# Performance work log

Measured on AMD Instinct MI355X. Metric: run time of the kernel, lower is better.

## Reference

```python
import jax, jax.numpy as jnp
import numpy as np

V, G, F, T = 500000, 25000, 256, 2


def setup_inputs() -> dict:
    key = jax.random.key(0)
    ks = jax.random.split(key, 10)
    s = 1.0 / np.sqrt(F)
    node_feats = jax.random.normal(ks[0], (V, F), jnp.float32)
    seg_ids = jnp.sort(jax.random.randint(ks[1], (V,), 0, G, dtype=jnp.int32))
    Wl = jax.random.uniform(ks[2], (T, 1, 2 * F), jnp.float32, -s, s)
    bl = jax.random.uniform(ks[3], (T, 1), jnp.float32, -s, s)
    Wp = jax.random.uniform(ks[4], (T, F, F), jnp.float32, -s, s)
    bp = jax.random.uniform(ks[5], (T, F), jnp.float32, -s, s)
    Wih = jax.random.uniform(ks[6], (T, 3 * F, F), jnp.float32, -s, s)
    Whh = jax.random.uniform(ks[7], (T, 3 * F, F), jnp.float32, -s, s)
    bih = jax.random.uniform(ks[8], (T, 3 * F), jnp.float32, -s, s)
    bhh = jax.random.uniform(ks[9], (T, 3 * F), jnp.float32, -s, s)
    return dict(node_feats=node_feats, seg_ids=seg_ids, Wl=Wl, bl=bl,
                Wp=Wp, bp=bp, Wih=Wih, Whh=Whh, bih=bih, bhh=bhh)


def _segment_softmax(z, seg):
    # z: (V,) per-node logits; softmax within each graph segment
    m = jax.ops.segment_max(z, seg, num_segments=G)
    m = jnp.where(jnp.isfinite(m), m, 0.0)  # guard empty segments
    e = jnp.exp(z - m[seg])
    d = jax.ops.segment_sum(e, seg, num_segments=G)
    return e / d[seg]


def _gru_cell(x, h, Wih, Whh, bih, bhh):
    # torch.nn.GRUCell semantics
    gi = x @ Wih.T + bih  # (G, 3F)
    gh = h @ Whh.T + bhh
    ir, iz, inn = jnp.split(gi, 3, axis=1)
    hr, hz, hn = jnp.split(gh, 3, axis=1)
    r = jax.nn.sigmoid(ir + hr)
    zg = jax.nn.sigmoid(iz + hz)
    n = jnp.tanh(inn + r * hn)
    return (1.0 - zg) * n + zg * h


def reference(node_feats, seg_ids, Wl, bl, Wp, bp, Wih, Whh, bih, bhh):
    # initial graph feats = sum of node feats per graph
    g_feats = jax.ops.segment_sum(node_feats, seg_ids, num_segments=G)  # (G, F)
    for t in range(T):
        ctx_in = jnp.concatenate([jax.nn.relu(g_feats)[seg_ids], node_feats], axis=1)  # (V, 2F)
        z = jax.nn.leaky_relu(ctx_in @ Wl[t].T + bl[t], 0.01)[:, 0]  # (V,)
        a = _segment_softmax(z, seg_ids)[:, None]  # (V, 1)
        hv = node_feats @ Wp[t].T + bp[t]  # dropout=0 -> identity
        g_repr = jax.ops.segment_sum(a * hv, seg_ids, num_segments=G)  # (G, F)
        context = jax.nn.elu(g_repr)
        g_feats = _gru_cell(context, g_feats, Wih[t], Whh[t], bih[t], bhh[t])
    return g_feats
```

## Files before the change

kernel.cpp:

```cpp
#include <hip/hip_runtime.h>
#include <cstdint>

typedef unsigned short u16;
typedef unsigned int u32;

#define V_N 500000
#define G_N 25000
#define F_N 256
#define GP_N 25088

typedef __attribute__((ext_vector_type(8))) __bf16 bf16x8;
typedef __attribute__((ext_vector_type(4))) float f32x4;

__device__ __forceinline__ u16 f2bf(float f) {
  u32 u = __builtin_bit_cast(u32, f);
  u += 0x7fffu + ((u >> 16) & 1u);
  return (u16)(u >> 16);
}
__device__ __forceinline__ float bf2f(u16 s) {
  u32 u = ((u32)s) << 16;
  return __builtin_bit_cast(float, u);
}
__device__ __forceinline__ float sigm(float x) { return 1.f / (1.f + __expf(-x)); }
__device__ __forceinline__ float tanh_fast(float x) {
  return 1.f - 2.f / (__expf(2.f * x) + 1.f);
}
__device__ __forceinline__ float lrelu(float z) { return z >= 0.f ? z : 0.01f * z; }

__device__ __forceinline__ void load_lds16(const void* g, void* l) {
  __builtin_amdgcn_global_load_lds(
      (const __attribute__((address_space(1))) void*)g,
      (__attribute__((address_space(3))) void*)l, 16, 0, 0);
}

__global__ __launch_bounds__(256) void k_convw(const float* __restrict__ Wp,
                                               const float* __restrict__ Wih,
                                               const float* __restrict__ Whh,
                                               u16* __restrict__ Wpb, u16* __restrict__ W3) {
  int i = blockIdx.x * 256 + threadIdx.x;
  const int NP = 2 * F_N * F_N;
  if (i < NP) {
    Wpb[i] = f2bf(Wp[i]);
    return;
  }
  int j = i - NP;
  int t = j >> 19;
  int r = j & 524287;
  int row = r >> 9;
  int k = r & 511;
  int q = row >> 6;
  int gate = (row >> 4) & 3;
  int c = q * 16 + (row & 15);
  const float* wi = Wih + t * 196608;
  const float* wh = Whh + t * 196608;
  float v;
  if (gate == 0) {
    v = (k < 256) ? wi[c * 256 + k] : wh[c * 256 + (k - 256)];
  } else if (gate == 1) {
    v = (k < 256) ? wi[(256 + c) * 256 + k] : wh[(256 + c) * 256 + (k - 256)];
  } else if (gate == 2) {
    v = (k < 256) ? wi[(512 + c) * 256 + k] : 0.f;
  } else {
    v = (k >= 256) ? wh[(512 + c) * 256 + (k - 256)] : 0.f;
  }
  W3[j] = f2bf(v);
}

__global__ __launch_bounds__(256) void k_offsets(const int* __restrict__ seg, int* __restrict__ off) {
  int v = blockIdx.x * 256 + threadIdx.x;
  if (v > V_N) return;
  if (v == 0) {
    int c = seg[0];
    for (int g = 0; g <= c; ++g) off[g] = 0;
  } else if (v == V_N) {
    int pr = seg[V_N - 1];
    for (int g = pr + 1; g <= G_N; ++g) off[g] = V_N;
  } else {
    int pr = seg[v - 1], c = seg[v];
    for (int g = pr + 1; g <= c; ++g) off[g] = v;
  }
}

__global__ __launch_bounds__(256) void k_node(const float* __restrict__ nf,
                                              const int* __restrict__ off,
                                              const float* __restrict__ Wl,
                                              u16* __restrict__ xb,
                                              float* __restrict__ q0, float* __restrict__ q1,
                                              float* __restrict__ hbuf0, u16* __restrict__ x2a,
                                              u16* __restrict__ x2b,
                                              u16* __restrict__ sb, float* __restrict__ Ag) {
  int g = blockIdx.x * 4 + (threadIdx.x >> 6);
  int lane = threadIdx.x & 63;
  if (g >= GP_N) return;
  if (g >= G_N) {
    float4 z4 = {0.f, 0.f, 0.f, 0.f};
    uint2 z2 = {0u, 0u};
    *reinterpret_cast<float4*>(hbuf0 + (size_t)g * F_N + lane * 4) = z4;
    *reinterpret_cast<uint2*>(x2a + (size_t)g * 512 + 256 + lane * 4) = z2;
    *reinterpret_cast<uint2*>(x2b + (size_t)g * 512 + 256 + lane * 4) = z2;
    *reinterpret_cast<uint2*>(sb + (size_t)g * F_N + lane * 4) = z2;
    if (lane == 0) Ag[g] = 0.f;
    return;
  }
  const float4 w0 = *reinterpret_cast<const float4*>(Wl + 256 + lane * 4);
  const float4 w1 = *reinterpret_cast<const float4*>(Wl + 768 + lane * 4);
  int s = off[g], e = off[g + 1];
  float a0 = 0.f, a1 = 0.f, a2 = 0.f, a3 = 0.f;
  for (int v = s; v < e; ++v) {
    const float4 x = *reinterpret_cast<const float4*>(nf + (size_t)v * F_N + lane * 4);
    a0 += x.x; a1 += x.y; a2 += x.z; a3 += x.w;
    uint2 pk;
    pk.x = (u32)f2bf(x.x) | ((u32)f2bf(x.y) << 16);
    pk.y = (u32)f2bf(x.z) | ((u32)f2bf(x.w) << 16);
    *reinterpret_cast<uint2*>(xb + (size_t)v * F_N + lane * 4) = pk;
    float d0 = x.x * w0.x + x.y * w0.y + x.z * w0.z + x.w * w0.w;
    float d1 = x.x * w1.x + x.y * w1.y + x.z * w1.z + x.w * w1.w;
#pragma unroll
    for (int m = 32; m >= 1; m >>= 1) {
      d0 += __shfl_xor(d0, m, 64);
      d1 += __shfl_xor(d1, m, 64);
    }
    if (lane == 0) {
      q0[v] = d0;
      q1[v] = d1;
    }
  }
  float4 h4 = {a0, a1, a2, a3};
  *reinterpret_cast<float4*>(hbuf0 + (size_t)g * F_N + lane * 4) = h4;
  uint2 hs;
  hs.x = (u32)f2bf(a0) | ((u32)f2bf(a1) << 16);
  hs.y = (u32)f2bf(a2) | ((u32)f2bf(a3) << 16);
  *reinterpret_cast<uint2*>(x2a + (size_t)g * 512 + 256 + lane * 4) = hs;
}

__global__ __launch_bounds__(256) void k_attn(const float* __restrict__ h,
                                              const u16* __restrict__ xb,
                                              const float* __restrict__ q,
                                              const int* __restrict__ off,
                                              const float* __restrict__ Wl,
                                              const float* __restrict__ bl, int t,
                                              u16* __restrict__ sb, float* __restrict__ Ag) {
  int g = blockIdx.x * 4 + (threadIdx.x >> 6);
  int lane = threadIdx.x & 63;
  if (g >= G_N) return;

  const float4 hv = *reinterpret_cast<const float4*>(h + (size_t)g * F_N + lane * 4);
  const float4 wv = *reinterpret_cast<const float4*>(Wl + t * 512 + lane * 4);
  float pd = fmaxf(hv.x, 0.f) * wv.x + fmaxf(hv.y, 0.f) * wv.y +
             fmaxf(hv.z, 0.f) * wv.z + fmaxf(hv.w, 0.f) * wv.w;
#pragma unroll
  for (int m = 32; m >= 1; m >>= 1) pd += __shfl_xor(pd, m, 64);
  float p = pd + bl[t];

  int s = off[g], n = off[g + 1] - s;
  if (n == 0) {
    if (lane < 32) {
      uint4 z = {0u, 0u, 0u, 0u};
      *reinterpret_cast<uint4*>(sb + (size_t)g * F_N + lane * 8) = z;
    }
    if (lane == 0) Ag[g] = 0.f;
    return;
  }
  float mloc = -3.4e38f;
  for (int i = lane; i < n; i += 64) mloc = fmaxf(mloc, lrelu(p + q[s + i]));
#pragma unroll
  for (int m = 32; m >= 1; m >>= 1) mloc = fmaxf(mloc, __shfl_xor(mloc, m, 64));
  float mx = mloc;
  float dloc = 0.f;
  for (int i = lane; i < n; i += 64) dloc += __expf(lrelu(p + q[s + i]) - mx);
#pragma unroll
  for (int m = 32; m >= 1; m >>= 1) dloc += __shfl_xor(dloc, m, 64);
  float inv = 1.f / dloc;

  int half = lane >> 5;
  int cl = (lane & 31) * 8;
  float acc[8] = {0.f, 0.f, 0.f, 0.f, 0.f, 0.f, 0.f, 0.f};
  for (int i = 0; i < n; i += 2) {
    int r = i + half;
    float a = 0.f;
    int row = s;
    if (r < n) {
      a = __expf(lrelu(p + q[s + r]) - mx) * inv;
      row = s + r;
    }
    uint4 x = *reinterpret_cast<const uint4*>(xb + (size_t)row * F_N + cl);
    acc[0] += a * bf2f((u16)(x.x & 0xffff));
    acc[1] += a * bf2f((u16)(x.x >> 16));
    acc[2] += a * bf2f((u16)(x.y & 0xffff));
    acc[3] += a * bf2f((u16)(x.y >> 16));
    acc[4] += a * bf2f((u16)(x.z & 0xffff));
    acc[5] += a * bf2f((u16)(x.z >> 16));
    acc[6] += a * bf2f((u16)(x.w & 0xffff));
    acc[7] += a * bf2f((u16)(x.w >> 16));
  }
#pragma unroll
  for (int k = 0; k < 8; ++k) acc[k] += __shfl_xor(acc[k], 32, 64);
  if (lane < 32) {
    uint4 o;
    o.x = (u32)f2bf(acc[0]) | ((u32)f2bf(acc[1]) << 16);
    o.y = (u32)f2bf(acc[2]) | ((u32)f2bf(acc[3]) << 16);
    o.z = (u32)f2bf(acc[4]) | ((u32)f2bf(acc[5]) << 16);
    o.w = (u32)f2bf(acc[6]) | ((u32)f2bf(acc[7]) << 16);
    *reinterpret_cast<uint4*>(sb + (size_t)g * F_N + cl) = o;
  }
  if (lane == 0) Ag[g] = 1.f;
}

__global__ __launch_bounds__(256) void k_gemm(const u16* __restrict__ A, const u16* __restrict__ B,
                                              int K, float* __restrict__ dst,
                                              u16* __restrict__ x2out, const float* __restrict__ AgH,
                                              const float* __restrict__ b1, const float* __restrict__ b2,
                                              int mode, int writehb) {
  __shared__ __align__(16) u16 As[128 * 64];
  __shared__ __align__(16) u16 Bs[128 * 64];
  int tid = threadIdx.x, lane = tid & 63, w = tid >> 6;
  int m0 = blockIdx.x * 128, n0 = blockIdx.y * 128;
  int wm = w >> 1, wn = w & 1;
  f32x4 zero = {0.f, 0.f, 0.f, 0.f};
  f32x4 acc[4][4];
#pragma unroll
  for (int i = 0; i < 4; ++i)
#pragma unroll
    for (int j = 0; j < 4; ++j) acc[i][j] = zero;

  int rowA = tid >> 3;
  int col8 = (tid & 7) * 8;
  for (int k0 = 0; k0 < K; k0 += 64) {
    __syncthreads();
#pragma unroll
    for (int c = 0; c < 4; ++c) {
      int r = c * 32 + rowA;
      const u16* gA = A + (size_t)(m0 + r) * K + k0 + col8;
      const u16* gB = B + (size_t)(n0 + r) * K + k0 + col8;
      char* lA = (char*)As + (c * 256 + w * 64) * 16;
      char* lB = (char*)Bs + (c * 256 + w * 64) * 16;
      load_lds16(gA, lA);
      load_lds16(gB, lB);
    }
    __syncthreads();
#pragma unroll
    for (int kk = 0; kk < 64; kk += 32) {
      bf16x8 af[4], bfr[4];
#pragma unroll
      for (int i = 0; i < 4; ++i) {
        af[i] = *reinterpret_cast<const bf16x8*>(&As[(wm * 64 + i * 16 + (lane & 15)) * 64 + kk + (lane >> 4) * 8]);
        bfr[i] = *reinterpret_cast<const bf16x8*>(&Bs[(wn * 64 + i * 16 + (lane & 15)) * 64 + kk + (lane >> 4) * 8]);
      }
#pragma unroll
      for (int i = 0; i < 4; ++i)
#pragma unroll
        for (int j = 0; j < 4; ++j)
          acc[i][j] = __builtin_amdgcn_mfma_f32_16x16x32_bf16(af[i], bfr[j], acc[i][j], 0, 0, 0);
    }
  }
  int crow0 = m0 + wm * 64 + (lane >> 4) * 4;
  if (mode == 1) {
    int ccol0 = n0 + wn * 64 + (lane & 15);
#pragma unroll
    for (int i = 0; i < 4; ++i)
#pragma unroll
      for (int j = 0; j < 4; ++j) {
        int col = ccol0 + j * 16;
#pragma unroll
        for (int r = 0; r < 4; ++r) {
          int row = crow0 + i * 16 + r;
          float v = acc[i][j][r] + AgH[row] * b1[col];
          v = v > 0.f ? v : (__expf(v) - 1.f);
          x2out[(size_t)row * 512 + col] = f2bf(v);
        }
      }
  } else {
    int qgrp = blockIdx.y * 2 + wn;
    int c = qgrp * 16 + (lane & 15);
    float bi0 = b1[c] + b2[c];
    float bi1 = b1[256 + c] + b2[256 + c];
    float bi2 = b1[512 + c];
    float bi3 = b2[512 + c];
#pragma unroll
    for (int i = 0; i < 4; ++i)
#pragma unroll
      for (int r = 0; r < 4; ++r) {
        int grow = crow0 + i * 16 + r;
        if (grow >= G_N) continue;
        float ir = acc[i][0][r] + bi0;
        float iz = acc[i][1][r] + bi1;
        float nn = acc[i][2][r] + bi2;
        float hn = acc[i][3][r] + bi3;
        float rg = sigm(ir);
        float zg = sigm(iz);
        float h0 = AgH[(size_t)grow * F_N + c];
        float nv = tanh_fast(nn + rg * hn);
        float hN = (1.f - zg) * nv + zg * h0;
        dst[(size_t)grow * F_N + c] = hN;
        if (writehb) x2out[(size_t)grow * 512 + 256 + c] = f2bf(hN);
      }
  }
}

extern "C" void kernel_launch(void* const* d_in, const int* in_sizes, int n_in,
                              void* d_out, int out_size, void* d_ws, size_t ws_size,
                              hipStream_t stream) {
  const float* nf = (const float*)d_in[0];
  const int* seg = (const int*)d_in[1];
  const float* Wl = (const float*)d_in[2];
  const float* bl = (const float*)d_in[3];
  const float* Wp = (const float*)d_in[4];
  const float* bp = (const float*)d_in[5];
  const float* Wih = (const float*)d_in[6];
  const float* Whh = (const float*)d_in[7];
  const float* bih = (const float*)d_in[8];
  const float* bhh = (const float*)d_in[9];
  float* out = (float*)d_out;

  char* p = (char*)d_ws;
  auto alloc = [&](size_t bytes) {
    char* r = p;
    p += (bytes + 511) & ~(size_t)511;
    return r;
  };
  float* q0 = (float*)alloc((size_t)V_N * 4);
  float* q1 = (float*)alloc((size_t)V_N * 4);
  int* off = (int*)alloc((size_t)(G_N + 1) * 4);
  float* hbuf0 = (float*)alloc((size_t)GP_N * F_N * 4);
  float* hbuf1 = (float*)alloc((size_t)GP_N * F_N * 4);
  u16* sb = (u16*)alloc((size_t)GP_N * F_N * 2);
  float* Ag = (float*)alloc((size_t)GP_N * 4);
  u16* X2a = (u16*)alloc((size_t)GP_N * 512 * 2);
  u16* X2b = (u16*)alloc((size_t)GP_N * 512 * 2);
  u16* Wpb = (u16*)alloc((size_t)2 * F_N * F_N * 2);
  u16* W3 = (u16*)alloc((size_t)2 * 1024 * 512 * 2);
  u16* xb = (u16*)alloc((size_t)V_N * F_N * 2);

  k_convw<<<4608, 256, 0, stream>>>(Wp, Wih, Whh, Wpb, W3);
  k_offsets<<<(V_N + 1 + 255) / 256, 256, 0, stream>>>(seg, off);
  k_node<<<GP_N / 4, 256, 0, stream>>>(nf, off, Wl, xb, q0, q1, hbuf0, X2a, X2b, sb, Ag);

  k_attn<<<G_N / 4, 256, 0, stream>>>(hbuf0, xb, q0, off, Wl, bl, 0, sb, Ag);
  k_gemm<<<dim3(GP_N / 128, 2), 256, 0, stream>>>(sb, Wpb, 256,
                                                  nullptr, X2a, Ag, bp, nullptr, 1, 0);
  k_gemm<<<dim3(GP_N / 128, 8), 256, 0, stream>>>(X2a, W3, 512,
                                                  hbuf1, X2b, hbuf0, bih, bhh, 2, 1);
  k_attn<<<G_N / 4, 256, 0, stream>>>(hbuf1, xb, q1, off, Wl, bl, 1, sb, Ag);
  k_gemm<<<dim3(GP_N / 128, 2), 256, 0, stream>>>(sb, Wpb + 65536, 256,
                                                  nullptr, X2b, Ag, bp + 256, nullptr, 1, 0);
  k_gemm<<<dim3(GP_N / 128, 8), 256, 0, stream>>>(X2b, W3 + 524288, 512,
                                                  out, nullptr, hbuf1, bih + 768, bhh + 768, 2, 0);
}
```

Baseline: 510.8 us.

## Fuse first attention step into node pass and merge prep kernels

Merges the weight-conversion and segment-offset kernels into a single launch, and folds the first-iteration attention (softmax and weighted bf16 sum) into the node-reduction kernel. The fused path reuses the segment sum already held in registers and keeps per-node logits in lanes for segments of up to 64 nodes. The node loop is unrolled by two so more loads are in flight. This removes two launches and the re-read of the segment sums. The trade-off is higher register pressure, plus a slow path for large segments that re-reads the logits.

```diff
diff --git a/kernel.cpp b/kernel.cpp
--- a/kernel.cpp
+++ b/kernel.cpp
@@ -33,10 +33,28 @@
       (__attribute__((address_space(3))) void*)l, 16, 0, 0);
 }
 
-__global__ __launch_bounds__(256) void k_convw(const float* __restrict__ Wp,
-                                               const float* __restrict__ Wih,
-                                               const float* __restrict__ Whh,
-                                               u16* __restrict__ Wpb, u16* __restrict__ W3) {
+#define CONVW_BLK 4608
+#define OFFS_BLK ((V_N + 1 + 255) / 256)
+__global__ __launch_bounds__(256) void k_prep(const float* __restrict__ Wp,
+                                              const float* __restrict__ Wih,
+                                              const float* __restrict__ Whh,
+                                              u16* __restrict__ Wpb, u16* __restrict__ W3,
+                                              const int* __restrict__ seg, int* __restrict__ off) {
+  if (blockIdx.x >= CONVW_BLK) {
+    int v = (blockIdx.x - CONVW_BLK) * 256 + threadIdx.x;
+    if (v > V_N) return;
+    if (v == 0) {
+      int c = seg[0];
+      for (int g = 0; g <= c; ++g) off[g] = 0;
+    } else if (v == V_N) {
+      int pr = seg[V_N - 1];
+      for (int g = pr + 1; g <= G_N; ++g) off[g] = V_N;
+    } else {
+      int pr = seg[v - 1], c = seg[v];
+      for (int g = pr + 1; g <= c; ++g) off[g] = v;
+    }
+    return;
+  }
   int i = blockIdx.x * 256 + threadIdx.x;
   const int NP = 2 * F_N * F_N;
   if (i < NP) {
@@ -66,29 +84,15 @@
   W3[j] = f2bf(v);
 }
 
-__global__ __launch_bounds__(256) void k_offsets(const int* __restrict__ seg, int* __restrict__ off) {
-  int v = blockIdx.x * 256 + threadIdx.x;
-  if (v > V_N) return;
-  if (v == 0) {
-    int c = seg[0];
-    for (int g = 0; g <= c; ++g) off[g] = 0;
-  } else if (v == V_N) {
-    int pr = seg[V_N - 1];
-    for (int g = pr + 1; g <= G_N; ++g) off[g] = V_N;
-  } else {
-    int pr = seg[v - 1], c = seg[v];
-    for (int g = pr + 1; g <= c; ++g) off[g] = v;
-  }
-}
-
-__global__ __launch_bounds__(256) void k_node(const float* __restrict__ nf,
-                                              const int* __restrict__ off,
-                                              const float* __restrict__ Wl,
-                                              u16* __restrict__ xb,
-                                              float* __restrict__ q0, float* __restrict__ q1,
-                                              float* __restrict__ hbuf0, u16* __restrict__ x2a,
-                                              u16* __restrict__ x2b,
-                                              u16* __restrict__ sb, float* __restrict__ Ag) {
+__global__ __launch_bounds__(256) void k_node_fused(const float* __restrict__ nf,
+                                                    const int* __restrict__ off,
+                                                    const float* __restrict__ Wl,
+                                                    const float* __restrict__ bl,
+                                                    u16* __restrict__ xb,
+                                                    float* __restrict__ q0, float* __restrict__ q1,
+                                                    float* __restrict__ hbuf0, u16* __restrict__ x2a,
+                                                    u16* __restrict__ x2b,
+                                                    u16* __restrict__ sb, float* __restrict__ Ag) {
   int g = blockIdx.x * 4 + (threadIdx.x >> 6);
   int lane = threadIdx.x & 63;
   if (g >= GP_N) return;
@@ -104,26 +108,58 @@
   }
   const float4 w0 = *reinterpret_cast<const float4*>(Wl + 256 + lane * 4);
   const float4 w1 = *reinterpret_cast<const float4*>(Wl + 768 + lane * 4);
+  const float4 wh = *reinterpret_cast<const float4*>(Wl + lane * 4);
   int s = off[g], e = off[g + 1];
+  int n = e - s;
   float a0 = 0.f, a1 = 0.f, a2 = 0.f, a3 = 0.f;
-  for (int v = s; v < e; ++v) {
-    const float4 x = *reinterpret_cast<const float4*>(nf + (size_t)v * F_N + lane * 4);
-    a0 += x.x; a1 += x.y; a2 += x.z; a3 += x.w;
-    uint2 pk;
-    pk.x = (u32)f2bf(x.x) | ((u32)f2bf(x.y) << 16);
-    pk.y = (u32)f2bf(x.z) | ((u32)f2bf(x.w) << 16);
-    *reinterpret_cast<uint2*>(xb + (size_t)v * F_N + lane * 4) = pk;
-    float d0 = x.x * w0.x + x.y * w0.y + x.z * w0.z + x.w * w0.w;
-    float d1 = x.x * w1.x + x.y * w1.y + x.z * w1.z + x.w * w1.w;
+  float qreg = 0.f;
+  int v = s;
+  for (; v + 2 <= e; v += 2) {
+    const float4 xA = *reinterpret_cast<const float4*>(nf + (size_t)v * F_N + lane * 4);
+    const float4 xB = *reinterpret_cast<const float4*>(nf + (size_t)(v + 1) * F_N + lane * 4);
+    a0 += xA.x + xB.x; a1 += xA.y + xB.y; a2 += xA.z + xB.z; a3 += xA.w + xB.w;
+    uint2 pA, pB;
+    pA.x = (u32)f2bf(xA.x) | ((u32)f2bf(xA.y) << 16);
+    pA.y = (u32)f2bf(xA.z) | ((u32)f2bf(xA.w) << 16);
+    pB.x = (u32)f2bf(xB.x) | ((u32)f2bf(xB.y) << 16);
+    pB.y = (u32)f2bf(xB.z) | ((u32)f2bf(xB.w) << 16);
+    *reinterpret_cast<uint2*>(xb + (size_t)v * F_N + lane * 4) = pA;
+    *reinterpret_cast<uint2*>(xb + (size_t)(v + 1) * F_N + lane * 4) = pB;
+    float dA0 = xA.x * w0.x + xA.y * w0.y + xA.z * w0.z + xA.w * w0.w;
+    float dA1 = xA.x * w1.x + xA.y * w1.y + xA.z * w1.z + xA.w * w1.w;
+    float dB0 = xB.x * w0.x + xB.y * w0.y + xB.z * w0.z + xB.w * w0.w;
+    float dB1 = xB.x * w1.x + xB.y * w1.y + xB.z * w1.z + xB.w * w1.w;
 #pragma unroll
     for (int m = 32; m >= 1; m >>= 1) {
-      d0 += __shfl_xor(d0, m, 64);
-      d1 += __shfl_xor(d1, m, 64);
+      dA0 += __shfl_xor(dA0, m, 64);
+      dA1 += __shfl_xor(dA1, m, 64);
+      dB0 += __shfl_xor(dB0, m, 64);
+      dB1 += __shfl_xor(dB1, m, 64);
     }
     if (lane == 0) {
-      q0[v] = d0;
-      q1[v] = d1;
-    }
+      q0[v] = dA0; q1[v] = dA1;
+      q0[v + 1] = dB0; q1[v + 1] = dB1;
+    }
+    int li = v - s;
+    if (li == lane) qreg = dA0;
+    if (li + 1 == lane) qreg = dB0;
+  }
+  if (v < e) {
+    const float4 xA = *reinterpret_cast<const float4*>(nf + (size_t)v * F_N + lane * 4);
+    a0 += xA.x; a1 += xA.y; a2 += xA.z; a3 += xA.w;
+    uint2 pA;
+    pA.x = (u32)f2bf(xA.x) | ((u32)f2bf(xA.y) << 16);
+    pA.y = (u32)f2bf(xA.z) | ((u32)f2bf(xA.w) << 16);
+    *reinterpret_cast<uint2*>(xb + (size_t)v * F_N + lane * 4) = pA;
+    float dA0 = xA.x * w0.x + xA.y * w0.y + xA.z * w0.z + xA.w * w0.w;
+    float dA1 = xA.x * w1.x + xA.y * w1.y + xA.z * w1.z + xA.w * w1.w;
+#pragma unroll
+    for (int m = 32; m >= 1; m >>= 1) {
+      dA0 += __shfl_xor(dA0, m, 64);
+      dA1 += __shfl_xor(dA1, m, 64);
+    }
+    if (lane == 0) { q0[v] = dA0; q1[v] = dA1; }
+    if (v - s == lane) qreg = dA0;
   }
   float4 h4 = {a0, a1, a2, a3};
   *reinterpret_cast<float4*>(hbuf0 + (size_t)g * F_N + lane * 4) = h4;
@@ -131,6 +167,83 @@
   hs.x = (u32)f2bf(a0) | ((u32)f2bf(a1) << 16);
   hs.y = (u32)f2bf(a2) | ((u32)f2bf(a3) << 16);
   *reinterpret_cast<uint2*>(x2a + (size_t)g * 512 + 256 + lane * 4) = hs;
+
+  if (n == 0) {
+    if (lane < 32) {
+      uint4 z = {0u, 0u, 0u, 0u};
+      *reinterpret_cast<uint4*>(sb + (size_t)g * F_N + lane * 8) = z;
+    }
+    if (lane == 0) Ag[g] = 0.f;
+    return;
+  }
+  float pd = fmaxf(a0, 0.f) * wh.x + fmaxf(a1, 0.f) * wh.y +
+             fmaxf(a2, 0.f) * wh.z + fmaxf(a3, 0.f) * wh.w;
+#pragma unroll
+  for (int m = 32; m >= 1; m >>= 1) pd += __shfl_xor(pd, m, 64);
+  float p = pd + bl[0];
+
+  float mx, inv, ee = 0.f;
+  bool fast = (n <= 64);
+  if (fast) {
+    float z = (lane < n) ? lrelu(p + qreg) : -3.4e38f;
+    float zm = z;
+#pragma unroll
+    for (int m = 32; m >= 1; m >>= 1) zm = fmaxf(zm, __shfl_xor(zm, m, 64));
+    mx = zm;
+    ee = (lane < n) ? __expf(z - mx) : 0.f;
+    float d = ee;
+#pragma unroll
+    for (int m = 32; m >= 1; m >>= 1) d += __shfl_xor(d, m, 64);
+    inv = 1.f / d;
+    asm volatile("s_waitcnt vmcnt(0)" ::: "memory");
+  } else {
+    asm volatile("s_waitcnt vmcnt(0)" ::: "memory");
+    float mloc = -3.4e38f;
+    for (int i = lane; i < n; i += 64) mloc = fmaxf(mloc, lrelu(p + q0[s + i]));
+#pragma unroll
+    for (int m = 32; m >= 1; m >>= 1) mloc = fmaxf(mloc, __shfl_xor(mloc, m, 64));
+    mx = mloc;
+    float dloc = 0.f;
+    for (int i = lane; i < n; i += 64) dloc += __expf(lrelu(p + q0[s + i]) - mx);
+#pragma unroll
+    for (int m = 32; m >= 1; m >>= 1) dloc += __shfl_xor(dloc, m, 64);
+    inv = 1.f / dloc;
+  }
+
+  int half = lane >> 5;
+  int cl = (lane & 31) * 8;
+  float acc[8] = {0.f, 0.f, 0.f, 0.f, 0.f, 0.f, 0.f, 0.f};
+  for (int i = 0; i < n; i += 2) {
+    int r = i + half;
+    float a;
+    if (fast) {
+      float ev = __shfl(ee, (r < 64 ? r : 63), 64);
+      a = (r < n) ? ev * inv : 0.f;
+    } else {
+      a = (r < n) ? __expf(lrelu(p + q0[s + r]) - mx) * inv : 0.f;
+    }
+    int row = s + (r < n ? r : 0);
+    uint4 x = *reinterpret_cast<const uint4*>(xb + (size_t)row * F_N + cl);
+    acc[0] += a * bf2f((u16)(x.x & 0xffff));
+    acc[1] += a * bf2f((u16)(x.x >> 16));
+    acc[2] += a * bf2f((u16)(x.y & 0xffff));
+    acc[3] += a * bf2f((u16)(x.y >> 16));
+    acc[4] += a * bf2f((u16)(x.z & 0xffff));
+    acc[5] += a * bf2f((u16)(x.z >> 16));
+    acc[6] += a * bf2f((u16)(x.w & 0xffff));
+    acc[7] += a * bf2f((u16)(x.w >> 16));
+  }
+#pragma unroll
+  for (int k = 0; k < 8; ++k) acc[k] += __shfl_xor(acc[k], 32, 64);
+  if (lane < 32) {
+    uint4 o;
+    o.x = (u32)f2bf(acc[0]) | ((u32)f2bf(acc[1]) << 16);
+    o.y = (u32)f2bf(acc[2]) | ((u32)f2bf(acc[3]) << 16);
+    o.z = (u32)f2bf(acc[4]) | ((u32)f2bf(acc[5]) << 16);
+    o.w = (u32)f2bf(acc[6]) | ((u32)f2bf(acc[7]) << 16);
+    *reinterpret_cast<uint4*>(sb + (size_t)g * F_N + cl) = o;
+  }
+  if (lane == 0) Ag[g] = 1.f;
 }
 
 __global__ __launch_bounds__(256) void k_attn(const float* __restrict__ h,
@@ -331,11 +444,10 @@
   u16* W3 = (u16*)alloc((size_t)2 * 1024 * 512 * 2);
   u16* xb = (u16*)alloc((size_t)V_N * F_N * 2);
 
-  k_convw<<<4608, 256, 0, stream>>>(Wp, Wih, Whh, Wpb, W3);
-  k_offsets<<<(V_N + 1 + 255) / 256, 256, 0, stream>>>(seg, off);
-  k_node<<<GP_N / 4, 256, 0, stream>>>(nf, off, Wl, xb, q0, q1, hbuf0, X2a, X2b, sb, Ag);
-
-  k_attn<<<G_N / 4, 256, 0, stream>>>(hbuf0, xb, q0, off, Wl, bl, 0, sb, Ag);
+  k_prep<<<CONVW_BLK + OFFS_BLK, 256, 0, stream>>>(Wp, Wih, Whh, Wpb, W3, seg, off);
+  k_node_fused<<<GP_N / 4, 256, 0, stream>>>(nf, off, Wl, bl, xb, q0, q1,
+                                             hbuf0, X2a, X2b, sb, Ag);
+
   k_gemm<<<dim3(GP_N / 128, 2), 256, 0, stream>>>(sb, Wpb, 256,
                                                   nullptr, X2a, Ag, bp, nullptr, 1, 0);
   k_gemm<<<dim3(GP_N / 128, 8), 256, 0, stream>>>(X2a, W3, 512,
```

New measurement: 467.2 us. 1.09x faster.
